# Optimization experiments

Measured on AMD Instinct MI355X. Metric: run time of the kernel, lower is better.

Reference implementation:

```python
import jax, jax.numpy as jnp
import numpy as np

D = 64      # latent dim (made.nin)
H = 512     # MADE hidden width

def _made_masks():
    # Standard MADE with sequential degrees (natural ordering).
    in_deg = np.arange(1, D + 1)                     # (D,)
    hid_deg = (np.arange(H) % (D - 1)) + 1           # (H,)
    out_deg = np.tile(in_deg, 2)                     # (2D,) mean+pre_scale share degrees
    M1 = (hid_deg[None, :] >= in_deg[:, None]).astype(np.float32)   # (D, H)
    M2 = (hid_deg[None, :] >= hid_deg[:, None]).astype(np.float32)  # (H, H)
    M3 = (out_deg[None, :] > hid_deg[:, None]).astype(np.float32)   # (H, 2D)
    return jnp.asarray(M1), jnp.asarray(M2), jnp.asarray(M3)

def setup_inputs() -> dict:
    key = jax.random.key(0)
    ks = jax.random.split(key, 8)
    B, S, C = 2048, 16, 256
    sc = 0.02
    return {
        'context': jax.random.normal(ks[0], (B, C), jnp.float32),
        'eps': jax.random.normal(ks[1], (S, B, D), jnp.float32),
        'W1': jax.random.normal(ks[2], (D, H), jnp.float32) * sc,
        'Wc': jax.random.normal(ks[3], (C, H), jnp.float32) * sc,
        'b1': jnp.zeros((H,), jnp.float32),
        'W2': jax.random.normal(ks[4], (H, H), jnp.float32) * sc,
        'b2': jnp.zeros((H,), jnp.float32),
        'W3': jax.random.normal(ks[5], (H, 2 * D), jnp.float32) * sc,
        'b3': jnp.zeros((2 * D,), jnp.float32),
    }

def reference(context, eps, W1, Wc, b1, W2, b2, W3, b3):
    M1, M2, M3 = _made_masks()
    S, B, _ = eps.shape
    ctx_proj = context @ Wc + b1                 # (B, H), constant across steps
    MW1, MW2, MW3 = M1 * W1, M2 * W2, M3 * W3

    def step(z, d):
        # z: (S, B, D) current partial sample
        h1 = jax.nn.relu(z @ MW1 + ctx_proj[None])          # (S, B, H)
        h2 = jax.nn.relu(h1 @ MW2 + b2)                     # (S, B, H)
        out = h2 @ MW3 + b3                                 # (S, B, 2D)
        mu, pre_scale = out[..., :D], out[..., D:]
        scale = jax.nn.softplus(pre_scale)
        onehot = jax.nn.one_hot(d, D, dtype=z.dtype)        # (D,)
        mu_d = (mu * onehot).sum(-1)                        # (S, B)
        scale_d = (scale * onehot).sum(-1)                  # (S, B)
        eps_d = (eps * onehot).sum(-1)                      # (S, B)
        z_d = mu_d + scale_d * eps_d                        # reparameterized Normal sample
        z = z + z_d[..., None] * onehot
        return z, (mu_d, scale_d)

    z0 = jnp.zeros((S, B, D), eps.dtype)
    z_samples, (mus, scales) = jax.lax.scan(step, z0, jnp.arange(D))
    mus = jnp.moveaxis(mus, 0, -1)       # (S, B, D)
    scales = jnp.moveaxis(scales, 0, -1) # (S, B, D)
    return z_samples, mus, scales
```

## Files before the change

kernel.cpp:

```cpp
#include <hip/hip_runtime.h>
#include <hip/hip_bf16.h>

#define ROWS 32
#define TPB 512

typedef unsigned short u16;
typedef __attribute__((ext_vector_type(8))) short bf16x8;
typedef __attribute__((ext_vector_type(16))) float f32x16;

__device__ __forceinline__ int deg_of_sorted(int i) {
  return (i < 72) ? (i / 9 + 1) : ((i - 8) / 8 + 1);
}
__device__ __forceinline__ int perm_of_sorted(int i) {
  int g, k;
  if (i < 72) { g = i / 9 + 1; k = i % 9; }
  else        { g = (i - 8) / 8 + 1; k = (i - 8) % 8; }
  return (g - 1) + 63 * k;
}
__device__ __forceinline__ int cum_deg(int d) {
  return (d <= 0) ? 0 : ((d <= 8) ? 9 * d : 8 * d + 8);
}
__device__ __forceinline__ u16 f2bfu(float x) {
  return __builtin_bit_cast(u16, __float2bfloat16(x));
}
__device__ __forceinline__ float softplus_f(float x) {
  return fmaxf(x, 0.f) + log1pf(expf(-fabsf(x)));
}

__global__ __launch_bounds__(256) void prep_w(
    const float* __restrict__ W1, const float* __restrict__ W2,
    const float* __restrict__ b2, const float* __restrict__ W3,
    float* __restrict__ mw1s, u16* __restrict__ mw2f,
    float* __restrict__ mw3f, float* __restrict__ b2s) {
  int idx = blockIdx.x * 256 + threadIdx.x;
  if (idx < 262144) {
    int kb = idx >> 12, n = (idx >> 3) & 511, kk = idx & 7;
    int k = kb * 8 + kk;
    float v = (deg_of_sorted(k) <= deg_of_sorted(n))
                  ? W2[perm_of_sorted(k) * 512 + perm_of_sorted(n)] : 0.f;
    mw2f[idx] = f2bfu(v);
    return;
  }
  idx -= 262144;
  if (idx < 32768) {
    int d = idx >> 9, j = idx & 511;
    mw1s[idx] = (deg_of_sorted(j) >= d + 1) ? W1[d * 512 + perm_of_sorted(j)] : 0.f;
    return;
  }
  idx -= 32768;
  if (idx < 65536) {
    int c = idx >> 9, j = idx & 511;
    mw3f[idx] = (deg_of_sorted(j) <= (c & 63)) ? W3[perm_of_sorted(j) * 128 + c] : 0.f;
    return;
  }
  idx -= 65536;
  if (idx < 512) b2s[idx] = b2[perm_of_sorted(idx)];
}

__global__ __launch_bounds__(256) void prep_ctx(
    const float* __restrict__ context, const float* __restrict__ Wc,
    const float* __restrict__ b1, float* __restrict__ ctxp) {
  __shared__ float cs[256];
  const int b = blockIdx.x;
  const int j = blockIdx.y * 256 + threadIdx.x;
  cs[threadIdx.x] = context[b * 256 + threadIdx.x];
  __syncthreads();
  const int pj = perm_of_sorted(j);
  float acc = b1[pj];
  #pragma unroll 4
  for (int c = 0; c < 256; ++c) acc += cs[c] * Wc[c * 512 + pj];
  ctxp[b * 512 + j] = acc;
}

__global__ __launch_bounds__(TPB, 4) void made_main(
    const float* __restrict__ eps, const float* __restrict__ b3,
    const float* __restrict__ ctxp, const float* __restrict__ mw1s,
    const float* __restrict__ mw3f, const float* __restrict__ b2sg,
    const u16* __restrict__ mw2f, float* __restrict__ out) {
  __shared__ __align__(16) u16   dbuf[2][32][32];
  __shared__ __align__(16) float part2mu[32 * 9];
  __shared__ __align__(16) float part2sc[32 * 9];
  __shared__ __align__(16) float w1s[512];
  __shared__ __align__(16) float w3fs[2][2][512];
  __shared__ __align__(16) float b3s[128];
  __shared__ __align__(16) float epsall[ROWS * 65];
  __shared__ __align__(16) float zLb[ROWS * 65];
  __shared__ __align__(16) float muLb[ROWS * 65];
  __shared__ __align__(16) float scLb[ROWS * 65];

  const int tid  = threadIdx.x;
  const int lane = tid & 63;
  const int wave = tid >> 6;
  const int g0   = blockIdx.x * ROWS;
  const int b0   = g0 & 2047;

  const int rA = tid & 31;
  const int jA = (tid >> 5) << 5;
  float a1r[32];
  #pragma unroll
  for (int t = 0; t < 8; ++t) {
    *(float4*)&a1r[t * 4] = *(const float4*)&ctxp[(b0 + rA) * 512 + jA + t * 4];
  }

  ((unsigned*)dbuf)[tid] = 0u;
  ((unsigned*)dbuf)[tid + 512] = 0u;
  if (tid < 128) b3s[tid] = b3[tid];
  {
    int r = tid >> 4, c = (tid & 15) * 4;
    float4 ev = *(const float4*)&eps[(g0 + r) * 64 + c];
    epsall[r * 65 + c + 0] = ev.x;
    epsall[r * 65 + c + 1] = ev.y;
    epsall[r * 65 + c + 2] = ev.z;
    epsall[r * 65 + c + 3] = ev.w;
  }
  if (tid < 256) {
    int c_sel = tid >> 7, j0 = (tid & 127) * 4;
    *(float4*)&w3fs[0][c_sel][j0] = *(const float4*)&mw3f[(c_sel * 64) * 512 + j0];
  }
  __syncthreads();

  const int m  = lane & 31;
  const int kq = lane >> 5;
  const int jt0 = wave;
  const int jt1 = 15 - wave;
  const u16* bLane = mw2f + ((kq * 512 + m) << 3);
  const u16* bp0   = bLane + jt0 * 256;
  const u16* bp1   = bLane + jt1 * 256;
  const int ke0full = cum_deg(deg_of_sorted(jt0 * 32 + 31));
  const int ke1full = cum_deg(deg_of_sorted(jt1 * 32 + 31));

  f32x16 acc0, acc1;
  #pragma unroll
  for (int i = 0; i < 16; ++i) {
    const int ni = (i & 3) + 8 * (i >> 2) + 4 * kq;
    acc0[i] = b2sg[jt0 * 32 + ni];
    acc1[i] = b2sg[jt1 * 32 + ni];
  }

  for (int d = 0; d < 64; ++d) {
    const int Cd    = cum_deg(d);
    const int Cnext = cum_deg(d + 1);
    const int Cprev = cum_deg(d - 1);
    const int cb    = d & 1;
    const int nb    = cb ^ 1;

    float4 w1stg;
    if (tid < 128) w1stg = *(const float4*)&mw1s[d * 512 + tid * 4];
    float4 w3stg;
    int c_sel = 0, j0 = 0;
    if (tid >= 128 && tid < 384 && d < 63) {
      int t2 = tid - 128;
      c_sel = t2 >> 7; j0 = (t2 & 127) * 4;
      w3stg = *(const float4*)&mw3f[(c_sel * 64 + d + 1) * 512 + j0];
    }

    if (d > 0) {
      const int kb  = Cprev >> 4;
      const int nks = ((Cd - 1) >> 4) - kb + 1;
      #pragma unroll 2
      for (int t = 0; t < nks; ++t) {
        const int ks = kb + t;
        bf16x8 dF = *(const bf16x8*)((const u16*)&dbuf[cb][m][0] + t * 16 + kq * 8);
        if (ke0full > ks * 16) {
          bf16x8 wA = *(const bf16x8*)(bp0 + ks * 8192);
          acc0 = __builtin_amdgcn_mfma_f32_32x32x16_bf16(wA, dF, acc0, 0, 0, 0);
        }
        if (ke1full > ks * 16) {
          bf16x8 wB = *(const bf16x8*)(bp1 + ks * 8192);
          acc1 = __builtin_amdgcn_mfma_f32_32x32x16_bf16(wB, dF, acc1, 0, 0, 0);
        }
      }
    }

    {
      const float* w3c = &w3fs[cb][0][0];
      float pmu = 0.f, psc = 0.f;
      #pragma unroll
      for (int g = 0; g < 4; ++g) {
        const int n0 = jt0 * 32 + 8 * g + 4 * kq;
        const int n1 = jt1 * 32 + 8 * g + 4 * kq;
        const float4 m0 = *(const float4*)&w3c[n0];
        const float4 s0 = *(const float4*)&w3c[512 + n0];
        const float4 m1 = *(const float4*)&w3c[n1];
        const float4 s1 = *(const float4*)&w3c[512 + n1];
        float h00 = fmaxf(acc0[4 * g + 0], 0.f), h10 = fmaxf(acc1[4 * g + 0], 0.f);
        float h01 = fmaxf(acc0[4 * g + 1], 0.f), h11 = fmaxf(acc1[4 * g + 1], 0.f);
        float h02 = fmaxf(acc0[4 * g + 2], 0.f), h12 = fmaxf(acc1[4 * g + 2], 0.f);
        float h03 = fmaxf(acc0[4 * g + 3], 0.f), h13 = fmaxf(acc1[4 * g + 3], 0.f);
        pmu += h00 * m0.x + h10 * m1.x;  psc += h00 * s0.x + h10 * s1.x;
        pmu += h01 * m0.y + h11 * m1.y;  psc += h01 * s0.y + h11 * s1.y;
        pmu += h02 * m0.z + h12 * m1.z;  psc += h02 * s0.z + h12 * s1.z;
        pmu += h03 * m0.w + h13 * m1.w;  psc += h03 * s0.w + h13 * s1.w;
      }
      pmu += __shfl_xor(pmu, 32);
      psc += __shfl_xor(psc, 32);
      if (kq == 0) {
        part2mu[m * 9 + wave] = pmu;
        part2sc[m * 9 + wave] = psc;
      }
    }

    ((unsigned*)dbuf[nb])[tid] = 0u;

    if (tid < 128) *(float4*)&w1s[tid * 4] = w1stg;
    else if (tid < 384 && d < 63) *(float4*)&w3fs[nb][c_sel][j0] = w3stg;
    __syncthreads();

    float msum = b3s[d], ssum = b3s[64 + d];
    #pragma unroll
    for (int w = 0; w < 8; ++w) {
      msum += part2mu[rA * 9 + w];
      ssum += part2sc[rA * 9 + w];
    }
    const float mu = msum;
    const float sc = softplus_f(ssum);
    const float z  = fmaf(sc, epsall[rA * 65 + d], mu);
    if (tid < 32) {
      zLb[rA * 65 + d]  = z;
      muLb[rA * 65 + d] = mu;
      scLb[rA * 65 + d] = sc;
    }

    if (jA + 31 >= Cd) {
      const int kbw = Cd >> 4;
      #pragma unroll
      for (int i = 0; i < 32; ++i) {
        int j = jA + i;
        if (j >= Cd) a1r[i] += z * w1s[j];
      }
      if (jA < Cnext) {
        #pragma unroll
        for (int i = 0; i < 32; ++i) {
          int j = jA + i;
          if (j >= Cd && j < Cnext) {
            dbuf[nb][rA][j - kbw * 16] = f2bfu(fmaxf(a1r[i], 0.f));
          }
        }
      }
    }
    __syncthreads();
  }

  {
    const int r = tid >> 4, c = (tid & 15) * 4;
    float4 zv, mv, sv;
    zv.x = zLb[r * 65 + c + 0]; zv.y = zLb[r * 65 + c + 1];
    zv.z = zLb[r * 65 + c + 2]; zv.w = zLb[r * 65 + c + 3];
    mv.x = muLb[r * 65 + c + 0]; mv.y = muLb[r * 65 + c + 1];
    mv.z = muLb[r * 65 + c + 2]; mv.w = muLb[r * 65 + c + 3];
    sv.x = scLb[r * 65 + c + 0]; sv.y = scLb[r * 65 + c + 1];
    sv.z = scLb[r * 65 + c + 2]; sv.w = scLb[r * 65 + c + 3];
    *(float4*)&out[(g0 + r) * 64 + c]           = zv;
    *(float4*)&out[2097152 + (g0 + r) * 64 + c] = mv;
    *(float4*)&out[4194304 + (g0 + r) * 64 + c] = sv;
  }
}

extern "C" void kernel_launch(void* const* d_in, const int* in_sizes, int n_in,
                              void* d_out, int out_size, void* d_ws, size_t ws_size,
                              hipStream_t stream) {
  (void)in_sizes; (void)n_in; (void)out_size; (void)ws_size;
  const float* context = (const float*)d_in[0];
  const float* eps     = (const float*)d_in[1];
  const float* W1      = (const float*)d_in[2];
  const float* Wc      = (const float*)d_in[3];
  const float* b1      = (const float*)d_in[4];
  const float* W2      = (const float*)d_in[5];
  const float* b2      = (const float*)d_in[6];
  const float* W3      = (const float*)d_in[7];
  const float* b3      = (const float*)d_in[8];
  float* out = (float*)d_out;

  float* ws   = (float*)d_ws;
  float* ctxp = ws;
  float* mw1s = ctxp + 1048576;
  float* b2s  = mw1s + 32768;
  float* mw3f = b2s + 512;
  u16*   mw2f = (u16*)(mw3f + 65536);

  prep_w<<<1410, 256, 0, stream>>>(W1, W2, b2, W3, mw1s, mw2f, mw3f, b2s);
  prep_ctx<<<dim3(2048, 2), 256, 0, stream>>>(context, Wc, b1, ctxp);
  made_main<<<1024, TPB, 0, stream>>>(eps, b3, ctxp, mw1s, mw3f, b2s, mw2f, out);
}
```

Measured before the change: 760.2 us.

## Tile context projection over rows, skip masked W3 tiles, transpose partial sums

```diff
diff --git a/kernel.cpp b/kernel.cpp
--- a/kernel.cpp
+++ b/kernel.cpp
@@ -57,19 +57,36 @@
   if (idx < 512) b2s[idx] = b2[perm_of_sorted(idx)];
 }
 
-__global__ __launch_bounds__(256) void prep_ctx(
+__global__ __launch_bounds__(512) void prep_ctx(
     const float* __restrict__ context, const float* __restrict__ Wc,
     const float* __restrict__ b1, float* __restrict__ ctxp) {
-  __shared__ float cs[256];
-  const int b = blockIdx.x;
-  const int j = blockIdx.y * 256 + threadIdx.x;
-  cs[threadIdx.x] = context[b * 256 + threadIdx.x];
+  __shared__ float cs[16][257];
+  const int tid = threadIdx.x;
+  const int b0  = blockIdx.x * 16;
+  for (int i = tid; i < 16 * 256; i += 512) {
+    int r = i >> 8, c = i & 255;
+    cs[r][c] = context[(b0 + r) * 256 + c];
+  }
   __syncthreads();
+  const int j  = tid;
   const int pj = perm_of_sorted(j);
-  float acc = b1[pj];
-  #pragma unroll 4
-  for (int c = 0; c < 256; ++c) acc += cs[c] * Wc[c * 512 + pj];
-  ctxp[b * 512 + j] = acc;
+  float acc[16];
+  const float bv = b1[pj];
+  #pragma unroll
+  for (int r = 0; r < 16; ++r) acc[r] = bv;
+  for (int c = 0; c < 256; c += 4) {
+    float w0 = Wc[(c + 0) * 512 + pj];
+    float w1 = Wc[(c + 1) * 512 + pj];
+    float w2 = Wc[(c + 2) * 512 + pj];
+    float w3 = Wc[(c + 3) * 512 + pj];
+    #pragma unroll
+    for (int r = 0; r < 16; ++r) {
+      acc[r] += cs[r][c + 0] * w0 + cs[r][c + 1] * w1 +
+                cs[r][c + 2] * w2 + cs[r][c + 3] * w3;
+    }
+  }
+  #pragma unroll
+  for (int r = 0; r < 16; ++r) ctxp[(b0 + r) * 512 + j] = acc[r];
 }
 
 __global__ __launch_bounds__(TPB, 4) void made_main(
@@ -78,8 +95,8 @@
     const float* __restrict__ mw3f, const float* __restrict__ b2sg,
     const u16* __restrict__ mw2f, float* __restrict__ out) {
   __shared__ __align__(16) u16   dbuf[2][32][32];
-  __shared__ __align__(16) float part2mu[32 * 9];
-  __shared__ __align__(16) float part2sc[32 * 9];
+  __shared__ __align__(16) float part2mu[9 * 33];
+  __shared__ __align__(16) float part2sc[9 * 33];
   __shared__ __align__(16) float w1s[512];
   __shared__ __align__(16) float w3fs[2][2][512];
   __shared__ __align__(16) float b3s[128];
@@ -175,28 +192,39 @@
     {
       const float* w3c = &w3fs[cb][0][0];
       float pmu = 0.f, psc = 0.f;
-      #pragma unroll
-      for (int g = 0; g < 4; ++g) {
-        const int n0 = jt0 * 32 + 8 * g + 4 * kq;
-        const int n1 = jt1 * 32 + 8 * g + 4 * kq;
-        const float4 m0 = *(const float4*)&w3c[n0];
-        const float4 s0 = *(const float4*)&w3c[512 + n0];
-        const float4 m1 = *(const float4*)&w3c[n1];
-        const float4 s1 = *(const float4*)&w3c[512 + n1];
-        float h00 = fmaxf(acc0[4 * g + 0], 0.f), h10 = fmaxf(acc1[4 * g + 0], 0.f);
-        float h01 = fmaxf(acc0[4 * g + 1], 0.f), h11 = fmaxf(acc1[4 * g + 1], 0.f);
-        float h02 = fmaxf(acc0[4 * g + 2], 0.f), h12 = fmaxf(acc1[4 * g + 2], 0.f);
-        float h03 = fmaxf(acc0[4 * g + 3], 0.f), h13 = fmaxf(acc1[4 * g + 3], 0.f);
-        pmu += h00 * m0.x + h10 * m1.x;  psc += h00 * s0.x + h10 * s1.x;
-        pmu += h01 * m0.y + h11 * m1.y;  psc += h01 * s0.y + h11 * s1.y;
-        pmu += h02 * m0.z + h12 * m1.z;  psc += h02 * s0.z + h12 * s1.z;
-        pmu += h03 * m0.w + h13 * m1.w;  psc += h03 * s0.w + h13 * s1.w;
+      if (jt0 * 32 < Cd) {
+        #pragma unroll
+        for (int g = 0; g < 4; ++g) {
+          const int n0 = jt0 * 32 + 8 * g + 4 * kq;
+          const float4 m0 = *(const float4*)&w3c[n0];
+          const float4 s0 = *(const float4*)&w3c[512 + n0];
+          float h0 = fmaxf(acc0[4 * g + 0], 0.f);
+          float h1 = fmaxf(acc0[4 * g + 1], 0.f);
+          float h2 = fmaxf(acc0[4 * g + 2], 0.f);
+          float h3 = fmaxf(acc0[4 * g + 3], 0.f);
+          pmu += h0 * m0.x + h1 * m0.y + h2 * m0.z + h3 * m0.w;
+          psc += h0 * s0.x + h1 * s0.y + h2 * s0.z + h3 * s0.w;
+        }
+      }
+      if (jt1 * 32 < Cd) {
+        #pragma unroll
+        for (int g = 0; g < 4; ++g) {
+          const int n1 = jt1 * 32 + 8 * g + 4 * kq;
+          const float4 m1 = *(const float4*)&w3c[n1];
+          const float4 s1 = *(const float4*)&w3c[512 + n1];
+          float h0 = fmaxf(acc1[4 * g + 0], 0.f);
+          float h1 = fmaxf(acc1[4 * g + 1], 0.f);
+          float h2 = fmaxf(acc1[4 * g + 2], 0.f);
+          float h3 = fmaxf(acc1[4 * g + 3], 0.f);
+          pmu += h0 * m1.x + h1 * m1.y + h2 * m1.z + h3 * m1.w;
+          psc += h0 * s1.x + h1 * s1.y + h2 * s1.z + h3 * s1.w;
+        }
       }
       pmu += __shfl_xor(pmu, 32);
       psc += __shfl_xor(psc, 32);
       if (kq == 0) {
-        part2mu[m * 9 + wave] = pmu;
-        part2sc[m * 9 + wave] = psc;
+        part2mu[wave * 33 + m] = pmu;
+        part2sc[wave * 33 + m] = psc;
       }
     }
 
@@ -209,8 +237,8 @@
     float msum = b3s[d], ssum = b3s[64 + d];
     #pragma unroll
     for (int w = 0; w < 8; ++w) {
-      msum += part2mu[rA * 9 + w];
-      ssum += part2sc[rA * 9 + w];
+      msum += part2mu[w * 33 + rA];
+      ssum += part2sc[w * 33 + rA];
     }
     const float mu = msum;
     const float sc = softplus_f(ssum);
@@ -279,6 +307,6 @@
   u16*   mw2f = (u16*)(mw3f + 65536);
 
   prep_w<<<1410, 256, 0, stream>>>(W1, W2, b2, W3, mw1s, mw2f, mw3f, b2s);
-  prep_ctx<<<dim3(2048, 2), 256, 0, stream>>>(context, Wc, b1, ctxp);
+  prep_ctx<<<128, 512, 0, stream>>>(context, Wc, b1, ctxp);
   made_main<<<1024, TPB, 0, stream>>>(eps, b3, ctxp, mw1s, mw3f, b2s, mw2f, out);
 }
```

After: 650.5 us. 14.4% less time.
